# Kernel tuning notes

Hardware: AMD Instinct MI355X
Metric: run time of the kernel (lower is better)

The kernel has to match this reference:

```python
import jax, jax.numpy as jnp
import numpy as np
from jax import lax

EDGES = [(11,12),(11,23),(12,24),(23,24),(23,25),(25,27),(24,26),(26,28),(11,13),(13,15),(12,14),(14,16)]
J = 33

def _build_neighbors():
    nb = [[j] for j in range(J)]
    for a, b in EDGES:
        nb[a].append(b); nb[b].append(a)
    K = max(len(n) for n in nb)
    idx = np.zeros((J, K), np.int32)
    msk = np.zeros((J, K), np.float32)
    for j, n in enumerate(nb):
        idx[j, :len(n)] = n; msk[j, :len(n)] = 1.0
    return jnp.asarray(idx), jnp.asarray(msk)

NBR_IDX, NBR_MASK = _build_neighbors()
BN_EPS = 1e-5

def conv(x, w, b):
    y = lax.conv_general_dilated(x, w, (1, 1), 'SAME', dimension_numbers=('NCHW', 'OIHW', 'NCHW'))
    return y + b[None, :, None, None]

def bn(x, g, b):
    # eval-mode BatchNorm with running_mean=0, running_var=1
    s = g / jnp.sqrt(1.0 + BN_EPS)
    return x * s[None, :, None, None] + b[None, :, None, None]

def maxpool2(x):
    return lax.reduce_window(x, -jnp.inf, lax.max, (1, 1, 2, 2), (1, 1, 2, 2), 'VALID')

def deconv2x2(x, w, b):
    # ConvTranspose2d(k=2, s=2): w is [Cin, Cout, 2, 2]
    y = jnp.einsum('bcij,codk->boidjk', x, w)
    B, O, H, _, W, _ = y.shape
    return y.reshape(B, O, 2 * H, 2 * W) + b[None, :, None, None]

def forward(x, conv1_w, conv1_b, bn1_g, bn1_b, conv2_w, conv2_b, bn2_g, bn2_b,
            conv3_w, conv3_b, bn3_g, bn3_b, conv4_w, conv4_b, bn4_g, bn4_b,
            dc1_w, dc1_b, dc2_w, dc2_b, head_w, head_b, proj_w, proj_b,
            msg_w, msg_b, gru_w_ih, gru_w_hh, gru_b_ih, gru_b_hh,
            refine_w, refine_b, vis_w1, vis_b1, vis_w2, vis_b2):
    relu = jax.nn.relu
    h = bn(relu(conv(x, conv1_w, conv1_b)), bn1_g, bn1_b)
    h = bn(relu(conv(h, conv2_w, conv2_b)), bn2_g, bn2_b)
    h = maxpool2(h)
    h = bn(relu(conv(h, conv3_w, conv3_b)), bn3_g, bn3_b)
    h = maxpool2(h)
    enc = bn(relu(conv(h, conv4_w, conv4_b)), bn4_g, bn4_b)  # [B,256,H/4,W/4]
    f = relu(deconv2x2(enc, dc1_w, dc1_b))
    feat_map = relu(deconv2x2(f, dc2_w, dc2_b))  # [B,64,H,W]
    init_hm = jax.nn.sigmoid(conv(feat_map, head_w, head_b))  # [B,J,H,W]
    B, Jn, H, W = init_hm.shape
    sm = jax.nn.softmax(init_hm.reshape(B, Jn, H * W) / 0.1, axis=-1).reshape(B, Jn, H, W)
    w_idx = jnp.linspace(0.0, 1.0, W)
    h_idx = jnp.linspace(0.0, 1.0, H)
    pred_x = (sm.sum(-2) * w_idx).sum(-1)  # [B,J] in [0,1]
    pred_y = (sm.sum(-1) * h_idx).sum(-1)
    # grid_sample bilinear, align_corners=True: grid=(2p-1) -> pixel coord p*(dim-1)
    ix = pred_x * (W - 1)
    iy = pred_y * (H - 1)
    x0 = jnp.clip(jnp.floor(ix), 0, W - 1)
    y0 = jnp.clip(jnp.floor(iy), 0, H - 1)
    wx = ix - x0
    wy = iy - y0
    x0i = x0.astype(jnp.int32); x1i = jnp.clip(x0i + 1, 0, W - 1)
    y0i = y0.astype(jnp.int32); y1i = jnp.clip(y0i + 1, 0, H - 1)
    fm = feat_map.transpose(0, 2, 3, 1)  # [B,H,W,C]
    bidx = jnp.arange(B)[:, None]
    v00 = fm[bidx, y0i, x0i]; v01 = fm[bidx, y0i, x1i]
    v10 = fm[bidx, y1i, x0i]; v11 = fm[bidx, y1i, x1i]
    wx = wx[..., None]; wy = wy[..., None]
    joint = (v00 * (1 - wx) * (1 - wy) + v01 * wx * (1 - wy)
             + v10 * (1 - wx) * wy + v11 * wx * wy)  # [B,J,64]
    joint_feats = joint @ proj_w.T + proj_b
    # SkeletonGNN (all joints read original joint_feats -> fully parallel)
    gathered = joint_feats[:, NBR_IDX, :]  # [B,J,K,D]
    lin = gathered @ msg_w.T + msg_b
    m = NBR_MASK[None, :, :, None]
    msgs = (lin * m).sum(2) / NBR_MASK.sum(1)[None, :, None]  # [B,J,D]
    gi = msgs @ gru_w_ih.T + gru_b_ih
    gh = joint_feats @ gru_w_hh.T + gru_b_hh
    D = joint_feats.shape[-1]
    ir, iz, inn = gi[..., :D], gi[..., D:2 * D], gi[..., 2 * D:]
    hr, hz, hn = gh[..., :D], gh[..., D:2 * D], gh[..., 2 * D:]
    r = jax.nn.sigmoid(ir + hr)
    z = jax.nn.sigmoid(iz + hz)
    n = jnp.tanh(inn + r * hn)
    refined_feats = (1 - z) * n + z * joint_feats
    refined_bias = refined_feats.mean(-1)[:, :, None, None]
    refined_hm = jax.nn.sigmoid(conv(init_hm, refine_w, refine_b) + refined_bias)
    # visibility head: adaptive avg pool to 4x4 (enc HW divisible by 4), eval dropout = identity
    eB, eC, eH, eW = enc.shape
    p = enc.reshape(eB, eC, 4, eH // 4, 4, eW // 4).mean((3, 5))  # [B,256,4,4]
    v = jax.nn.relu(p.reshape(eB, -1) @ vis_w1.T + vis_b1)
    vis_pred = jax.nn.sigmoid(v @ vis_w2.T + vis_b2)
    return refined_hm, vis_pred

def setup_inputs() -> dict:
    key = jax.random.key(0)
    ks = iter(jax.random.split(key, 64))
    def w(shape, s=0.05):
        return (jax.random.normal(next(ks), shape, dtype=jnp.float32) * s)
    inp = {
        'x': jax.random.normal(next(ks), (16, 3, 256, 256), dtype=jnp.float32),
        'conv1_w': w((32, 3, 3, 3)), 'conv1_b': w((32,)), 'bn1_g': jnp.ones((32,)), 'bn1_b': jnp.zeros((32,)),
        'conv2_w': w((64, 32, 3, 3)), 'conv2_b': w((64,)), 'bn2_g': jnp.ones((64,)), 'bn2_b': jnp.zeros((64,)),
        'conv3_w': w((128, 64, 3, 3)), 'conv3_b': w((128,)), 'bn3_g': jnp.ones((128,)), 'bn3_b': jnp.zeros((128,)),
        'conv4_w': w((256, 128, 3, 3)), 'conv4_b': w((256,)), 'bn4_g': jnp.ones((256,)), 'bn4_b': jnp.zeros((256,)),
        'dc1_w': w((256, 128, 2, 2)), 'dc1_b': w((128,)),
        'dc2_w': w((128, 64, 2, 2)), 'dc2_b': w((64,)),
        'head_w': w((33, 64, 1, 1)), 'head_b': w((33,)),
        'proj_w': w((64, 64)), 'proj_b': w((64,)),
        'msg_w': w((64, 64)), 'msg_b': w((64,)),
        'gru_w_ih': w((192, 64)), 'gru_w_hh': w((192, 64)),
        'gru_b_ih': w((192,)), 'gru_b_hh': w((192,)),
        'refine_w': w((33, 33, 3, 3)), 'refine_b': w((33,)),
        'vis_w1': w((256, 256 * 16)), 'vis_b1': w((256,)),
        'vis_w2': w((33, 256)), 'vis_b2': w((33,)),
    }
    return inp

def reference(x, conv1_w, conv1_b, bn1_g, bn1_b, conv2_w, conv2_b, bn2_g, bn2_b,
              conv3_w, conv3_b, bn3_g, bn3_b, conv4_w, conv4_b, bn4_g, bn4_b,
              dc1_w, dc1_b, dc2_w, dc2_b, head_w, head_b, proj_w, proj_b,
              msg_w, msg_b, gru_w_ih, gru_w_hh, gru_b_ih, gru_b_hh,
              refine_w, refine_b, vis_w1, vis_b1, vis_w2, vis_b2):
    return forward(x, conv1_w, conv1_b, bn1_g, bn1_b, conv2_w, conv2_b, bn2_g, bn2_b,
                   conv3_w, conv3_b, bn3_g, bn3_b, conv4_w, conv4_b, bn4_g, bn4_b,
                   dc1_w, dc1_b, dc2_w, dc2_b, head_w, head_b, proj_w, proj_b,
                   msg_w, msg_b, gru_w_ih, gru_w_hh, gru_b_ih, gru_b_hh,
                   refine_w, refine_b, vis_w1, vis_b1, vis_w2, vis_b2)
```

## Files before the change

### kernel.cpp

```cpp
#include <hip/hip_runtime.h>
#include <hip/hip_bf16.h>
#include <math.h>

#define BN_RS 0.99999500003749977f

typedef __attribute__((ext_vector_type(8))) __bf16 bf16x8;
typedef __attribute__((ext_vector_type(4))) float f32x4;

union U16 { uint4 u; bf16x8 v; __hip_bfloat16 h[8]; };
union U8  { uint2 u; __hip_bfloat16 h[4]; };

__device__ __forceinline__ float sigf(float v) { return 1.0f / (1.0f + expf(-v)); }

__global__ __launch_bounds__(256)
void repack_conv_w_k(const float* __restrict__ w, __hip_bfloat16* __restrict__ wb,
                     int taps, int Co, int Ci, int CoT, int Kp)
{
    int i = blockIdx.x * 256 + threadIdx.x;
    int tot = taps * CoT * Kp;
    if (i >= tot) return;
    int k = i % Kp, n = (i / Kp) % CoT, t = i / (Kp * CoT);
    float v = (n < Co && k < Ci) ? w[((long)n * Ci + k) * taps + t] : 0.0f;
    wb[i] = __float2bfloat16(v);
}
__global__ __launch_bounds__(256)
void repack_conv_w_ilv_k(const float* __restrict__ w, __hip_bfloat16* __restrict__ wb,
                         int taps, int Co, int Ci, int CoT, int Kp)
{
    int i = blockIdx.x * 256 + threadIdx.x;
    int tot = taps * CoT * Kp;
    if (i >= tot) return;
    int k = i % Kp, n = (i / Kp) % CoT, t = i / (Kp * CoT);
    int grp = n >> 6, r = n & 63;
    int c = (grp << 6) + (r & 15) * 4 + (r >> 4);
    float v = (c < Co && k < Ci) ? w[((long)c * Ci + k) * taps + t] : 0.0f;
    wb[i] = __float2bfloat16(v);
}
__global__ __launch_bounds__(256)
void repack_deconv_w_ilv_k(const float* __restrict__ w, __hip_bfloat16* __restrict__ wb,
                           int Co, int Ci)
{
    int i = blockIdx.x * 256 + threadIdx.x;
    int tot = 4 * Co * Ci;
    if (i >= tot) return;
    int k = i % Ci, n = (i / Ci) % Co, q = i / (Ci * Co);
    int grp = n >> 6, r = n & 63;
    int c = (grp << 6) + (r & 15) * 4 + (r >> 4);
    wb[i] = __float2bfloat16(w[((long)k * Co + c) * 4 + q]);
}

__global__ __launch_bounds__(256)
void zero_halo_k(__hip_bfloat16* __restrict__ buf, int H, int W, int C, int B)
{
    const int P = W + 2;
    const long per = (long)(2 * P + 2 * H) * C;
    long idx = (long)blockIdx.x * 256 + threadIdx.x;
    if (idx >= per * B) return;
    int b = (int)(idx / per);
    long r = idx % per;
    long off;
    if (r < (long)2 * P * C) {
        int row = (r >= (long)P * C) ? (H + 1) : 0;
        long r2 = r % ((long)P * C);
        off = (((long)b * (H + 2) + row) * P) * C + r2;
    } else {
        long r2 = r - (long)2 * P * C;
        int row = 1 + (int)(r2 / (2 * C));
        int side = (int)((r2 / C) & 1);
        int ch = (int)(r2 % C);
        off = (((long)b * (H + 2) + row) * P + (side ? (W + 1) : 0)) * C + ch;
    }
    buf[off] = __float2bfloat16(0.0f);
}

__global__ __launch_bounds__(256)
void conv1_k(const float* __restrict__ x, const float* __restrict__ w,
             const float* __restrict__ cb, const float* __restrict__ g,
             const float* __restrict__ bb, __hip_bfloat16* __restrict__ out)
{
    __shared__ float sw[216];
    const int tid = threadIdx.x;
    const int b = blockIdx.z >> 2, cg = blockIdx.z & 3, co0 = cg * 8;
    for (int i = tid; i < 216; i += 256) {
        int t = i % 9, co = (i / 9) % 8, ci = i / 72;
        sw[i] = w[((co0 + co) * 3 + ci) * 9 + t];
    }
    __syncthreads();
    const int tx = tid & 15, ty = tid >> 4;
    const int y = blockIdx.y * 16 + ty;
    const int xs = blockIdx.x * 64 + tx;
    float acc[4][8];
#pragma unroll
    for (int p = 0; p < 4; ++p)
#pragma unroll
        for (int c = 0; c < 8; ++c) acc[p][c] = 0.0f;
    for (int ci = 0; ci < 3; ++ci) {
        const float* plane = x + ((long)b * 3 + ci) * 65536;
#pragma unroll
        for (int t = 0; t < 9; ++t) {
            const int dy = t / 3 - 1, dx = t % 3 - 1;
            const int yy = y + dy;
            if ((unsigned)yy < 256u) {
                const float* row = plane + yy * 256;
                float wsr[8];
#pragma unroll
                for (int c = 0; c < 8; ++c) wsr[c] = sw[ci * 72 + c * 9 + t];
#pragma unroll
                for (int p = 0; p < 4; ++p) {
                    const int xx = xs + p * 16 + dx;
                    const float v = ((unsigned)xx < 256u) ? row[xx] : 0.0f;
#pragma unroll
                    for (int c = 0; c < 8; ++c) acc[p][c] = fmaf(v, wsr[c], acc[p][c]);
                }
            }
        }
    }
#pragma unroll
    for (int p = 0; p < 4; ++p) {
        U16 o;
#pragma unroll
        for (int c = 0; c < 8; ++c) {
            const int cc = co0 + c;
            float v = fmaxf(acc[p][c] + cb[cc], 0.0f) * (g[cc] * BN_RS) + bb[cc];
            o.h[c] = __float2bfloat16(v);
        }
        *(uint4*)(void*)(out + ((long)b * 2130048L + ((long)y * 258 + xs + p * 16) * 32) + co0) = o.u;
    }
}

template<int MI>
__global__ __launch_bounds__(256)
void mfma_conv_k(const __hip_bfloat16* __restrict__ in,
                 const __hip_bfloat16* __restrict__ wb,
                 const float* __restrict__ cbias,
                 const float* __restrict__ bng, const float* __restrict__ bnb,
                 __hip_bfloat16* __restrict__ out_bf,
                 int H, int W, int Cin, int PIT, long bstride, long obstride, int OPIT,
                 int CoutT, int CG, int S)
{
    const int tid = threadIdx.x;
    const int wid = tid >> 6, lane = tid & 63;
    const int ln = lane & 15, kg = lane >> 4;
    const int nx = gridDim.x;
    const int bx = (blockIdx.x & 7) * (nx >> 3) + (blockIdx.x >> 3);
    const int u = bx * 4 + wid;
    const int y = u / S, x0 = (u % S) * (MI * 16);
    const int b = blockIdx.z / CG, cg = blockIdx.z % CG;
    const int co0 = cg * 64;
    const int KC = Cin >> 5;

    f32x4 acc[MI][4];
#pragma unroll
    for (int i = 0; i < MI; ++i)
#pragma unroll
        for (int j = 0; j < 4; ++j) acc[i][j] = f32x4{0.f, 0.f, 0.f, 0.f};

    for (int kc = 0; kc < KC; ++kc) {
        const int kofs = kc * 32 + kg * 8;
#pragma unroll
        for (int t = 0; t < 9; ++t) {
            const int dy = t / 3 - 1, dx = t % 3 - 1;
            bf16x8 wfr[4];
#pragma unroll
            for (int ni = 0; ni < 4; ++ni)
                wfr[ni] = *(const bf16x8*)(const void*)(wb + ((long)t * CoutT + co0 + ni * 16 + ln) * Cin + kofs);
            U16 av[MI];
            const long rowb = (long)b * bstride + (long)(y + dy) * PIT * Cin + kofs;
#pragma unroll
            for (int mi = 0; mi < MI; ++mi)
                av[mi].u = *(const uint4*)(const void*)(in + rowb + (long)(x0 + mi * 16 + ln + dx) * Cin);
#pragma unroll
            for (int mi = 0; mi < MI; ++mi)
#pragma unroll
                for (int ni = 0; ni < 4; ++ni)
                    acc[mi][ni] = __builtin_amdgcn_mfma_f32_16x16x32_bf16(av[mi].v, wfr[ni], acc[mi][ni], 0, 0, 0);
        }
    }
#pragma unroll
    for (int mi = 0; mi < MI; ++mi) {
#pragma unroll
        for (int r = 0; r < 4; ++r) {
            const int px = x0 + mi * 16 + kg * 4 + r;
            const long pb = (long)b * obstride + ((long)y * OPIT + px) * CoutT + co0;
            U8 o;
#pragma unroll
            for (int ni = 0; ni < 4; ++ni) {
                const int c = co0 + ln * 4 + ni;
                float v = acc[mi][ni][r] + cbias[c];
                v = fmaxf(v, 0.0f) * (bng[c] * BN_RS) + bnb[c];
                o.h[ni] = __float2bfloat16(v);
            }
            *(uint2*)(void*)(out_bf + pb + ln * 4) = o.u;
        }
    }
}

__global__ __launch_bounds__(256)
void mfma_deconv_k(const __hip_bfloat16* __restrict__ in,
                   const __hip_bfloat16* __restrict__ wb,
                   const float* __restrict__ bias,
                   __hip_bfloat16* __restrict__ out,
                   int H, int W, int Cin, int CoutT, int CG, int S)
{
    const int tid = threadIdx.x;
    const int wid = tid >> 6, lane = tid & 63;
    const int ln = lane & 15, kg = lane >> 4;
    const int nx = gridDim.x;
    const int bx = (blockIdx.x & 7) * (nx >> 3) + (blockIdx.x >> 3);
    const int u = bx * 4 + wid;
    const int y = u / S, x0 = (u % S) * 32;
    const int b = blockIdx.z / CG, cg = blockIdx.z % CG;
    const int co0 = cg * 64;
    const int KC = Cin >> 5;
    const long inb = (long)b * H * W * Cin;
    const int W2 = W * 2;
    const long ob = (long)b * 4 * H * W * CoutT;

    for (int q = 0; q < 4; ++q) {
        const int dy = q >> 1, dx = q & 1;
        f32x4 acc[2][4];
#pragma unroll
        for (int i = 0; i < 2; ++i)
#pragma unroll
            for (int j = 0; j < 4; ++j) acc[i][j] = f32x4{0.f, 0.f, 0.f, 0.f};
        for (int kc = 0; kc < KC; ++kc) {
            const int kofs = kc * 32 + kg * 8;
            bf16x8 wfr[4];
            U16 av[2];
#pragma unroll
            for (int ni = 0; ni < 4; ++ni)
                wfr[ni] = *(const bf16x8*)(const void*)(wb + ((long)q * CoutT + co0 + ni * 16 + ln) * Cin + kofs);
#pragma unroll
            for (int mi = 0; mi < 2; ++mi)
                av[mi].u = *(const uint4*)(const void*)(in + inb + ((long)y * W + x0 + mi * 16 + ln) * Cin + kofs);
#pragma unroll
            for (int mi = 0; mi < 2; ++mi)
#pragma unroll
                for (int ni = 0; ni < 4; ++ni)
                    acc[mi][ni] = __builtin_amdgcn_mfma_f32_16x16x32_bf16(av[mi].v, wfr[ni], acc[mi][ni], 0, 0, 0);
        }
#pragma unroll
        for (int mi = 0; mi < 2; ++mi) {
#pragma unroll
            for (int r = 0; r < 4; ++r) {
                const int xl = x0 + mi * 16 + kg * 4 + r;
                const long pb = ob + ((long)(2 * y + dy) * W2 + 2 * xl + dx) * CoutT + co0;
                U8 o;
#pragma unroll
                for (int ni = 0; ni < 4; ++ni) {
                    const int c = co0 + ln * 4 + ni;
                    float v = fmaxf(acc[mi][ni][r] + bias[c], 0.0f);
                    o.h[ni] = __float2bfloat16(v);
                }
                *(uint2*)(void*)(out + pb + ln * 4) = o.u;
            }
        }
    }
}

__global__ __launch_bounds__(256)
void mfma_head_k(const __hip_bfloat16* __restrict__ in,
                 const __hip_bfloat16* __restrict__ wb,
                 const float* __restrict__ hb,
                 __hip_bfloat16* __restrict__ out)
{
    const int tid = threadIdx.x;
    const int wid = tid >> 6, lane = tid & 63;
    const int ln = lane & 15, kg = lane >> 4;
    const int nx = gridDim.x;
    const int bx = (blockIdx.x & 7) * (nx >> 3) + (blockIdx.x >> 3);
    const int u = bx * 4 + wid;
    const int y = u >> 3, x0 = (u & 7) * 32;
    const int b = blockIdx.z;

    f32x4 acc[2][4];
#pragma unroll
    for (int i = 0; i < 2; ++i)
#pragma unroll
        for (int j = 0; j < 4; ++j) acc[i][j] = f32x4{0.f, 0.f, 0.f, 0.f};

    for (int kc = 0; kc < 2; ++kc) {
        const int kofs = kc * 32 + kg * 8;
        bf16x8 wfr[4];
#pragma unroll
        for (int ni = 0; ni < 4; ++ni)
            wfr[ni] = *(const bf16x8*)(const void*)(wb + ((long)(ni * 16 + ln)) * 64 + kofs);
        U16 av[2];
#pragma unroll
        for (int mi = 0; mi < 2; ++mi)
            av[mi].u = *(const uint4*)(const void*)(in + (long)b * 4194304L + ((long)y * 256 + x0 + mi * 16 + ln) * 64 + kofs);
#pragma unroll
        for (int mi = 0; mi < 2; ++mi)
#pragma unroll
            for (int ni = 0; ni < 4; ++ni)
                acc[mi][ni] = __builtin_amdgcn_mfma_f32_16x16x32_bf16(av[mi].v, wfr[ni], acc[mi][ni], 0, 0, 0);
    }
#pragma unroll
    for (int mi = 0; mi < 2; ++mi) {
#pragma unroll
        for (int r = 0; r < 4; ++r) {
            const int px = x0 + mi * 16 + kg * 4 + r;
            const long pb = (long)b * 4260096L + ((long)y * 258 + px) * 64;
            U8 o;
#pragma unroll
            for (int ni = 0; ni < 4; ++ni) {
                const int c = ln * 4 + ni;
                float v = (c < 33) ? sigf(acc[mi][ni][r] + hb[c]) : 0.0f;
                o.h[ni] = __float2bfloat16(v);
            }
            *(uint2*)(void*)(out + pb + ln * 4) = o.u;
        }
    }
}

__global__ __launch_bounds__(256)
void mfma_refine_k(const __hip_bfloat16* __restrict__ in,
                   const __hip_bfloat16* __restrict__ wb,
                   const float* __restrict__ cbias, const float* __restrict__ ebias,
                   float* __restrict__ out_f32)
{
    extern __shared__ float ltr[];
    const int tid = threadIdx.x;
    const int wid = tid >> 6, lane = tid & 63;
    const int ln = lane & 15, kg = lane >> 4;
    const int nx = gridDim.x;
    const int bx = (blockIdx.x & 7) * (nx >> 3) + (blockIdx.x >> 3);
    const int u = bx * 4 + wid;
    const int y = u >> 3, x0 = (u & 7) * 32;
    const int b = blockIdx.z;

    f32x4 acc[2][3];
#pragma unroll
    for (int i = 0; i < 2; ++i)
#pragma unroll
        for (int j = 0; j < 3; ++j) acc[i][j] = f32x4{0.f, 0.f, 0.f, 0.f};

    for (int kc = 0; kc < 2; ++kc) {
        const int kofs = kc * 32 + kg * 8;
#pragma unroll
        for (int t = 0; t < 9; ++t) {
            const int dy = t / 3 - 1, dx = t % 3 - 1;
            bf16x8 wfr[3];
#pragma unroll
            for (int ni = 0; ni < 3; ++ni)
                wfr[ni] = *(const bf16x8*)(const void*)(wb + ((long)t * 64 + ni * 16 + ln) * 64 + kofs);
            U16 av[2];
            const long rowb = (long)b * 4260096L + (long)(y + dy) * 258 * 64 + kofs;
#pragma unroll
            for (int mi = 0; mi < 2; ++mi)
                av[mi].u = *(const uint4*)(const void*)(in + rowb + (long)(x0 + mi * 16 + ln + dx) * 64);
#pragma unroll
            for (int mi = 0; mi < 2; ++mi)
#pragma unroll
                for (int ni = 0; ni < 3; ++ni)
                    acc[mi][ni] = __builtin_amdgcn_mfma_f32_16x16x32_bf16(av[mi].v, wfr[ni], acc[mi][ni], 0, 0, 0);
        }
    }

    float* wt = ltr + wid * 1680;
#pragma unroll
    for (int mi = 0; mi < 2; ++mi) {
#pragma unroll
        for (int r = 0; r < 4; ++r) {
            const int pxl = mi * 16 + kg * 4 + r;
#pragma unroll
            for (int ni = 0; ni < 3; ++ni) {
                const int c = ni * 16 + ln;
                float eb = (c < 33) ? (cbias[c] + ebias[b * 33 + c]) : 0.0f;
                wt[c * 35 + pxl] = sigf(acc[mi][ni][r] + eb);
            }
        }
    }
    __syncthreads();
    const int yb = (bx * 4) >> 3;
    const int xb = ((bx * 4) & 7) * 32;
    const int coff = bx % 33;
    for (int i = tid; i < 4224; i += 256) {
        int cl = i >> 7, p = i & 127;
        int c = cl + coff; if (c >= 33) c -= 33;
        float v = ltr[(p >> 5) * 1680 + c * 35 + (p & 31)];
        out_f32[((long)b * 33 + c) * 65536L + (long)yb * 256 + xb + p] = v;
    }
}

__global__ __launch_bounds__(256)
void maxpool_bf_k(const __hip_bfloat16* __restrict__ in, __hip_bfloat16* __restrict__ out,
                  int Ho, int Wo, int C, long total, int OPIT, long obstride)
{
    long idx = (long)blockIdx.x * 256 + threadIdx.x;
    if (idx >= total) return;
    const int ng = C >> 3;
    const int cg = (int)(idx % ng);
    long pix = idx / ng;
    const int xo = (int)(pix % Wo); pix /= Wo;
    const int yo = (int)(pix % Ho);
    const int b = (int)(pix / Ho);
    const int Wi = Wo * 2;
    const __hip_bfloat16* p = in + (((long)b * 2 * Ho + 2 * yo) * Wi + 2 * xo) * C + cg * 8;
    U16 a0, a1, a2, a3, o;
    a0.u = *(const uint4*)(const void*)p;
    a1.u = *(const uint4*)(const void*)(p + C);
    a2.u = *(const uint4*)(const void*)(p + (long)Wi * C);
    a3.u = *(const uint4*)(const void*)(p + (long)Wi * C + C);
#pragma unroll
    for (int j = 0; j < 8; ++j) {
        float m = fmaxf(fmaxf(__bfloat162float(a0.h[j]), __bfloat162float(a1.h[j])),
                        fmaxf(__bfloat162float(a2.h[j]), __bfloat162float(a3.h[j])));
        o.h[j] = __float2bfloat16(m);
    }
    *(uint4*)(void*)(out + (long)b * obstride + ((long)yo * OPIT + xo) * C + cg * 8) = o.u;
}

__global__ __launch_bounds__(256)
void softargmax_nhwc_k(const __hip_bfloat16* __restrict__ hd, float* __restrict__ coords)
{
    __shared__ float sm[8][256];
    __shared__ float fin[8][4];
    const int b = blockIdx.x, jg = blockIdx.y;
    const int tid = threadIdx.x;
    const __hip_bfloat16* base = hd + (long)b * 4260096L + jg * 8;
    float m[8];
#pragma unroll
    for (int c = 0; c < 8; ++c) m[c] = -1e30f;
    for (int i = tid; i < 65536; i += 256) {
        int y = i >> 8, x = i & 255;
        U16 v; v.u = *(const uint4*)(const void*)(base + ((long)y * 258 + x) * 64);
#pragma unroll
        for (int c = 0; c < 8; ++c) m[c] = fmaxf(m[c], __bfloat162float(v.h[c]));
    }
#pragma unroll
    for (int c = 0; c < 8; ++c) sm[c][tid] = m[c];
    __syncthreads();
    for (int s = 128; s > 0; s >>= 1) {
        if (tid < s)
#pragma unroll
            for (int c = 0; c < 8; ++c) sm[c][tid] = fmaxf(sm[c][tid], sm[c][tid + s]);
        __syncthreads();
    }
    if (tid < 8) fin[tid][0] = sm[tid][0];
    __syncthreads();
#pragma unroll
    for (int c = 0; c < 8; ++c) m[c] = fin[c][0];
    float s8[8], sx8[8], sy8[8];
#pragma unroll
    for (int c = 0; c < 8; ++c) { s8[c] = 0.f; sx8[c] = 0.f; sy8[c] = 0.f; }
    for (int i = tid; i < 65536; i += 256) {
        int y = i >> 8, x = i & 255;
        U16 v; v.u = *(const uint4*)(const void*)(base + ((long)y * 258 + x) * 64);
#pragma unroll
        for (int c = 0; c < 8; ++c) {
            float e = expf((__bfloat162float(v.h[c]) - m[c]) * 10.0f);
            s8[c] += e; sx8[c] += e * (float)x; sy8[c] += e * (float)y;
        }
    }
    for (int which = 0; which < 3; ++which) {
        __syncthreads();
#pragma unroll
        for (int c = 0; c < 8; ++c)
            sm[c][tid] = (which == 0) ? s8[c] : (which == 1) ? sx8[c] : sy8[c];
        __syncthreads();
        for (int s = 128; s > 0; s >>= 1) {
            if (tid < s)
#pragma unroll
                for (int c = 0; c < 8; ++c) sm[c][tid] += sm[c][tid + s];
            __syncthreads();
        }
        if (tid < 8) fin[tid][1 + which] = sm[tid][0];
    }
    __syncthreads();
    if (tid < 8) {
        int j = jg * 8 + tid;
        if (j < 33) {
            coords[2 * (b * 33 + j)]     = fin[tid][2] / fin[tid][1];
            coords[2 * (b * 33 + j) + 1] = fin[tid][3] / fin[tid][1];
        }
    }
}

__global__ __launch_bounds__(64)
void joint_bf_k(const __hip_bfloat16* __restrict__ fm, const float* __restrict__ coords,
                const float* __restrict__ pw, const float* __restrict__ pb,
                float* __restrict__ jf)
{
    __shared__ float sj[64];
    const int bj = blockIdx.x, b = bj / 33;
    const int tid = threadIdx.x;
    float ix = coords[2 * bj], iy = coords[2 * bj + 1];
    float x0f = fminf(fmaxf(floorf(ix), 0.0f), 255.0f);
    float y0f = fminf(fmaxf(floorf(iy), 0.0f), 255.0f);
    float wx = ix - x0f, wy = iy - y0f;
    int x0 = (int)x0f, y0 = (int)y0f;
    int x1 = min(x0 + 1, 255), y1 = min(y0 + 1, 255);
    const __hip_bfloat16* base = fm + (long)b * 65536 * 64 + tid;
    float v00 = __bfloat162float(base[((long)y0 * 256 + x0) * 64]);
    float v01 = __bfloat162float(base[((long)y0 * 256 + x1) * 64]);
    float v10 = __bfloat162float(base[((long)y1 * 256 + x0) * 64]);
    float v11 = __bfloat162float(base[((long)y1 * 256 + x1) * 64]);
    sj[tid] = v00 * (1 - wx) * (1 - wy) + v01 * wx * (1 - wy)
            + v10 * (1 - wx) * wy + v11 * wx * wy;
    __syncthreads();
    float a = pb[tid];
    for (int k = 0; k < 64; ++k) a = fmaf(sj[k], pw[tid * 64 + k], a);
    jf[(long)bj * 64 + tid] = a;
}

__device__ const int d_nbr[33][4] = {
    {0,0,0,0},{1,0,0,0},{2,0,0,0},{3,0,0,0},{4,0,0,0},{5,0,0,0},{6,0,0,0},{7,0,0,0},
    {8,0,0,0},{9,0,0,0},{10,0,0,0},
    {11,12,23,13},{12,11,24,14},{13,11,15,0},{14,12,16,0},{15,13,0,0},{16,14,0,0},
    {17,0,0,0},{18,0,0,0},{19,0,0,0},{20,0,0,0},{21,0,0,0},{22,0,0,0},
    {23,11,24,25},{24,12,23,26},{25,23,27,0},{26,24,28,0},{27,25,0,0},{28,26,0,0},
    {29,0,0,0},{30,0,0,0},{31,0,0,0},{32,0,0,0}};
__device__ const int d_cnt[33] = {1,1,1,1,1,1,1,1,1,1,1,4,4,3,3,2,2,1,1,1,1,1,1,4,4,3,3,2,2,1,1,1,1};

__global__ __launch_bounds__(192)
void gru_k(const float* __restrict__ jf, const float* __restrict__ mw, const float* __restrict__ mb,
           const float* __restrict__ wih, const float* __restrict__ whh,
           const float* __restrict__ bih, const float* __restrict__ bhh,
           float* __restrict__ rbias)
{
    __shared__ float s_mjf[64], s_jf[64], s_msg[64], s_gi[192], s_gh[192], s_ref[64];
    const int bj = blockIdx.x;
    const int b = bj / 33, j = bj % 33;
    const int tid = threadIdx.x;
    if (tid < 64) {
        int cnt = d_cnt[j];
        float s = 0.0f;
        for (int n = 0; n < 4; ++n)
            if (n < cnt) s += jf[((long)b * 33 + d_nbr[j][n]) * 64 + tid];
        s_mjf[tid] = s / (float)cnt;
        s_jf[tid] = jf[(long)bj * 64 + tid];
    }
    __syncthreads();
    if (tid < 64) {
        float a = mb[tid];
        for (int k = 0; k < 64; ++k) a = fmaf(mw[tid * 64 + k], s_mjf[k], a);
        s_msg[tid] = a;
    }
    __syncthreads();
    {
        float a = bih[tid], c = bhh[tid];
        for (int k = 0; k < 64; ++k) {
            a = fmaf(wih[tid * 64 + k], s_msg[k], a);
            c = fmaf(whh[tid * 64 + k], s_jf[k], c);
        }
        s_gi[tid] = a; s_gh[tid] = c;
    }
    __syncthreads();
    if (tid < 64) {
        float r = sigf(s_gi[tid] + s_gh[tid]);
        float z = sigf(s_gi[64 + tid] + s_gh[64 + tid]);
        float n = tanhf(s_gi[128 + tid] + r * s_gh[128 + tid]);
        s_ref[tid] = (1.0f - z) * n + z * s_jf[tid];
    }
    __syncthreads();
    if (tid == 0) {
        float s = 0.0f;
        for (int k = 0; k < 64; ++k) s += s_ref[k];
        rbias[bj] = s * (1.0f / 64.0f);
    }
}

__global__ __launch_bounds__(256)
void vispool_bf_k(const __hip_bfloat16* __restrict__ enc, float* __restrict__ p)
{
    int idx = blockIdx.x * 256 + threadIdx.x;
    int v = idx & 3, uu = (idx >> 2) & 3, c = (idx >> 4) & 255, b = idx >> 12;
    const __hip_bfloat16* base = enc + (long)b * 64 * 64 * 256 + c;
    float s = 0.0f;
    for (int a = 0; a < 16; ++a)
#pragma unroll
        for (int d = 0; d < 16; ++d)
            s += __bfloat162float(base[((long)(uu * 16 + a) * 64 + (v * 16 + d)) * 256]);
    p[idx] = s * (1.0f / 256.0f);
}

__global__ __launch_bounds__(256)
void visfc1_k(const float* __restrict__ p, const float* __restrict__ w1,
              const float* __restrict__ b1, float* __restrict__ v1)
{
    __shared__ float s_p[4096];
    const int b = blockIdx.x, tid = threadIdx.x;
    for (int i = tid; i < 4096; i += 256) s_p[i] = p[b * 4096 + i];
    __syncthreads();
    float a = b1[tid];
    const float* wr = w1 + (long)tid * 4096;
    for (int k = 0; k < 4096; ++k) a = fmaf(wr[k], s_p[k], a);
    v1[b * 256 + tid] = fmaxf(a, 0.0f);
}

__global__ __launch_bounds__(64)
void visfc2_k(const float* __restrict__ v1, const float* __restrict__ w2,
              const float* __restrict__ b2, float* __restrict__ out)
{
    const int b = blockIdx.x, t = threadIdx.x;
    if (t < 33) {
        float a = b2[t];
        for (int k = 0; k < 256; ++k) a = fmaf(w2[t * 256 + k], v1[b * 256 + k], a);
        out[b * 33 + t] = sigf(a);
    }
}

extern "C" void kernel_launch(void* const* d_in, const int* in_sizes, int n_in,
                              void* d_out, int out_size, void* d_ws, size_t ws_size,
                              hipStream_t stream)
{
    const float* x   = (const float*)d_in[0];
    const float* c1w = (const float*)d_in[1];  const float* c1b = (const float*)d_in[2];
    const float* b1g = (const float*)d_in[3];  const float* b1b = (const float*)d_in[4];
    const float* c2w = (const float*)d_in[5];  const float* c2b = (const float*)d_in[6];
    const float* b2g = (const float*)d_in[7];  const float* b2b = (const float*)d_in[8];
    const float* c3w = (const float*)d_in[9];  const float* c3b = (const float*)d_in[10];
    const float* b3g = (const float*)d_in[11]; const float* b3b = (const float*)d_in[12];
    const float* c4w = (const float*)d_in[13]; const float* c4b = (const float*)d_in[14];
    const float* b4g = (const float*)d_in[15]; const float* b4b = (const float*)d_in[16];
    const float* d1w = (const float*)d_in[17]; const float* d1b = (const float*)d_in[18];
    const float* d2w = (const float*)d_in[19]; const float* d2b = (const float*)d_in[20];
    const float* hw  = (const float*)d_in[21]; const float* hb  = (const float*)d_in[22];
    const float* pw  = (const float*)d_in[23]; const float* pb  = (const float*)d_in[24];
    const float* mw  = (const float*)d_in[25]; const float* mb  = (const float*)d_in[26];
    const float* wih = (const float*)d_in[27]; const float* whh = (const float*)d_in[28];
    const float* bih = (const float*)d_in[29]; const float* bhh = (const float*)d_in[30];
    const float* rw  = (const float*)d_in[31]; const float* rb  = (const float*)d_in[32];
    const float* v1w = (const float*)d_in[33]; const float* v1b = (const float*)d_in[34];
    const float* v2w = (const float*)d_in[35]; const float* v2b = (const float*)d_in[36];

    char* ws = (char*)d_ws;
    __hip_bfloat16* ENC  = (__hip_bfloat16*)(ws + 0L);
    __hip_bfloat16* R1   = (__hip_bfloat16*)(ws + 33554432L);
    __hip_bfloat16* R2   = (__hip_bfloat16*)(ws + 167772160L);
    char*           R3c  = ws + 304095232L;
    char* SM = ws + 442507264L;

    __hip_bfloat16* H1B = R1;                 __hip_bfloat16* H1I = R1 + 8288;
    __hip_bfloat16* P1B = R1;                 __hip_bfloat16* P1I = R1 + 8384;
    __hip_bfloat16* FEAT = R1;
    __hip_bfloat16* H3  = R2;
    __hip_bfloat16* F   = R2;
    __hip_bfloat16* HDB = R2;                 __hip_bfloat16* HDI = R2 + 16576;
    __hip_bfloat16* P2B = (__hip_bfloat16*)R3c; __hip_bfloat16* P2I = P2B + 8576;

    __hip_bfloat16* W2B = (__hip_bfloat16*)(SM + 0);
    __hip_bfloat16* W3B = (__hip_bfloat16*)(SM + 36864);
    __hip_bfloat16* W4B = (__hip_bfloat16*)(SM + 184320);
    __hip_bfloat16* WRB = (__hip_bfloat16*)(SM + 774144);
    __hip_bfloat16* WHB = (__hip_bfloat16*)(SM + 847872);
    __hip_bfloat16* WD1 = (__hip_bfloat16*)(SM + 856064);
    __hip_bfloat16* WD2 = (__hip_bfloat16*)(SM + 1118208);
    float* CO = (float*)(SM + 1183744);
    float* JF = (float*)(SM + 1187968);
    float* RB = (float*)(SM + 1323136);
    float* P  = (float*)(SM + 1325248);
    float* V1 = (float*)(SM + 1587392);

    float* out_hm  = (float*)d_out;
    float* out_vis = out_hm + 34603008L;
    __hip_bfloat16* H2 = (__hip_bfloat16*)d_out;

    repack_conv_w_ilv_k<<<(9*64*32 + 255)/256, 256, 0, stream>>>(c2w, W2B, 9, 64, 32, 64, 32);
    repack_conv_w_ilv_k<<<(9*128*64 + 255)/256, 256, 0, stream>>>(c3w, W3B, 9, 128, 64, 128, 64);
    repack_conv_w_ilv_k<<<(9*256*128 + 255)/256, 256, 0, stream>>>(c4w, W4B, 9, 256, 128, 256, 128);
    repack_conv_w_k<<<(9*64*64 + 255)/256, 256, 0, stream>>>(rw, WRB, 9, 33, 33, 64, 64);
    repack_conv_w_ilv_k<<<(1*64*64 + 255)/256, 256, 0, stream>>>(hw, WHB, 1, 33, 64, 64, 64);
    repack_deconv_w_ilv_k<<<(4*128*256 + 255)/256, 256, 0, stream>>>(d1w, WD1, 128, 256);
    repack_deconv_w_ilv_k<<<(4*64*128 + 255)/256, 256, 0, stream>>>(d2w, WD2, 64, 128);

    zero_halo_k<<<(526336 + 255)/256, 256, 0, stream>>>(H1B, 256, 256, 32, 16);
    zero_halo_k<<<(532480 + 255)/256, 256, 0, stream>>>(P2B, 64, 64, 128, 16);

    conv1_k<<<dim3(4, 16, 64), 256, 0, stream>>>(x, c1w, c1b, b1g, b1b, H1I);
    mfma_conv_k<2><<<dim3(512, 1, 16), 256, 0, stream>>>(
        H1I, W2B, c2b, b2g, b2b, H2,
        256, 256, 32, 258, 2130048L, 4194304L, 256, 64, 1, 8);
    zero_halo_k<<<(528384 + 255)/256, 256, 0, stream>>>(P1B, 128, 128, 64, 16);
    maxpool_bf_k<<<8192, 256, 0, stream>>>(H2, P1I, 128, 128, 64, 2097152L, 130, 1081600L);
    mfma_conv_k<2><<<dim3(128, 1, 32), 256, 0, stream>>>(
        P1I, W3B, c3b, b3g, b3b, H3,
        128, 128, 64, 130, 1081600L, 2097152L, 128, 128, 2, 4);
    maxpool_bf_k<<<4096, 256, 0, stream>>>(H3, P2I, 64, 64, 128, 1048576L, 66, 557568L);
    mfma_conv_k<2><<<dim3(32, 1, 64), 256, 0, stream>>>(
        P2I, W4B, c4b, b4g, b4b, ENC,
        64, 64, 128, 66, 557568L, 1048576L, 64, 256, 4, 2);
    mfma_deconv_k<<<dim3(32, 1, 32), 256, 0, stream>>>(
        ENC, WD1, d1b, F, 64, 64, 256, 128, 2, 2);
    mfma_deconv_k<<<dim3(128, 1, 16), 256, 0, stream>>>(
        F, WD2, d2b, FEAT, 128, 128, 128, 64, 1, 4);
    zero_halo_k<<<(1052672 + 255)/256, 256, 0, stream>>>(HDB, 256, 256, 64, 16);
    mfma_head_k<<<dim3(512, 1, 16), 256, 0, stream>>>(FEAT, WHB, hb, HDI);
    softargmax_nhwc_k<<<dim3(16, 5), 256, 0, stream>>>(HDI, CO);
    joint_bf_k<<<528, 64, 0, stream>>>(FEAT, CO, pw, pb, JF);
    gru_k<<<528, 192, 0, stream>>>(JF, mw, mb, wih, whh, bih, bhh, RB);
    mfma_refine_k<<<dim3(512, 1, 16), 256, 26880, stream>>>(
        HDI, WRB, rb, RB, out_hm);
    vispool_bf_k<<<256, 256, 0, stream>>>(ENC, P);
    visfc1_k<<<16, 256, 0, stream>>>(P, v1w, v1b, V1);
    visfc2_k<<<16, 64, 0, stream>>>(V1, v2w, v2b, out_vis);
}
```

Measured before the change: 1.856 ms.

## Split soft-argmax into per-slab partial reductions plus a combine kernel

```diff
diff --git a/kernel.cpp b/kernel.cpp
--- a/kernel.cpp
+++ b/kernel.cpp
@@ -412,69 +412,96 @@
 }
 
 __global__ __launch_bounds__(256)
-void softargmax_nhwc_k(const __hip_bfloat16* __restrict__ hd, float* __restrict__ coords)
-{
-    __shared__ float sm[8][256];
-    __shared__ float fin[8][4];
-    const int b = blockIdx.x, jg = blockIdx.y;
+void softargmax_slab_k(const __hip_bfloat16* __restrict__ hd, float* __restrict__ ss)
+{
+    __shared__ float sm[64 * 33];
+    __shared__ float mg[64];
+    const int blk = blockIdx.x;
+    const int b = blk >> 4, slab = blk & 15;
     const int tid = threadIdx.x;
-    const __hip_bfloat16* base = hd + (long)b * 4260096L + jg * 8;
-    float m[8];
-#pragma unroll
-    for (int c = 0; c < 8; ++c) m[c] = -1e30f;
-    for (int i = tid; i < 65536; i += 256) {
-        int y = i >> 8, x = i & 255;
-        U16 v; v.u = *(const uint4*)(const void*)(base + ((long)y * 258 + x) * 64);
-#pragma unroll
-        for (int c = 0; c < 8; ++c) m[c] = fmaxf(m[c], __bfloat162float(v.h[c]));
-    }
-#pragma unroll
-    for (int c = 0; c < 8; ++c) sm[c][tid] = m[c];
-    __syncthreads();
-    for (int s = 128; s > 0; s >>= 1) {
-        if (tid < s)
-#pragma unroll
-            for (int c = 0; c < 8; ++c) sm[c][tid] = fmaxf(sm[c][tid], sm[c][tid + s]);
+    const int pxl = tid >> 3, cg = tid & 7;
+    const __hip_bfloat16* base = hd + (long)b * 4260096L + (long)(slab * 16) * 258 * 64 + cg * 8;
+
+    float m8[8];
+#pragma unroll
+    for (int c = 0; c < 8; ++c) m8[c] = -1e30f;
+    for (int yy = 0; yy < 16; ++yy)
+        for (int xc = 0; xc < 8; ++xc) {
+            U16 v; v.u = *(const uint4*)(const void*)(base + ((long)yy * 258 + xc * 32 + pxl) * 64);
+#pragma unroll
+            for (int c = 0; c < 8; ++c) m8[c] = fmaxf(m8[c], __bfloat162float(v.h[c]));
+        }
+#pragma unroll
+    for (int c = 0; c < 8; ++c) sm[(cg * 8 + c) * 33 + pxl] = m8[c];
+    __syncthreads();
+    for (int s = 16; s > 0; s >>= 1) {
+        if (pxl < s)
+#pragma unroll
+            for (int c = 0; c < 8; ++c) {
+                int a = (cg * 8 + c) * 33;
+                sm[a + pxl] = fmaxf(sm[a + pxl], sm[a + pxl + s]);
+            }
         __syncthreads();
     }
-    if (tid < 8) fin[tid][0] = sm[tid][0];
-    __syncthreads();
-#pragma unroll
-    for (int c = 0; c < 8; ++c) m[c] = fin[c][0];
+    if (tid < 64) mg[tid] = sm[tid * 33];
+    __syncthreads();
+    if (tid < 33) ss[(long)blk * 132 + tid] = mg[tid];
+    float mm[8];
+#pragma unroll
+    for (int c = 0; c < 8; ++c) mm[c] = mg[cg * 8 + c];
+
     float s8[8], sx8[8], sy8[8];
 #pragma unroll
     for (int c = 0; c < 8; ++c) { s8[c] = 0.f; sx8[c] = 0.f; sy8[c] = 0.f; }
-    for (int i = tid; i < 65536; i += 256) {
-        int y = i >> 8, x = i & 255;
-        U16 v; v.u = *(const uint4*)(const void*)(base + ((long)y * 258 + x) * 64);
-#pragma unroll
-        for (int c = 0; c < 8; ++c) {
-            float e = expf((__bfloat162float(v.h[c]) - m[c]) * 10.0f);
-            s8[c] += e; sx8[c] += e * (float)x; sy8[c] += e * (float)y;
+    for (int yy = 0; yy < 16; ++yy) {
+        const float fy = (float)(slab * 16 + yy);
+        for (int xc = 0; xc < 8; ++xc) {
+            const int x = xc * 32 + pxl;
+            U16 v; v.u = *(const uint4*)(const void*)(base + ((long)yy * 258 + x) * 64);
+#pragma unroll
+            for (int c = 0; c < 8; ++c) {
+                float e = expf((__bfloat162float(v.h[c]) - mm[c]) * 10.0f);
+                s8[c] += e; sx8[c] += e * (float)x; sy8[c] += e * fy;
+            }
         }
     }
     for (int which = 0; which < 3; ++which) {
         __syncthreads();
 #pragma unroll
         for (int c = 0; c < 8; ++c)
-            sm[c][tid] = (which == 0) ? s8[c] : (which == 1) ? sx8[c] : sy8[c];
+            sm[(cg * 8 + c) * 33 + pxl] = (which == 0) ? s8[c] : (which == 1) ? sx8[c] : sy8[c];
         __syncthreads();
-        for (int s = 128; s > 0; s >>= 1) {
-            if (tid < s)
-#pragma unroll
-                for (int c = 0; c < 8; ++c) sm[c][tid] += sm[c][tid + s];
+        for (int s = 16; s > 0; s >>= 1) {
+            if (pxl < s)
+#pragma unroll
+                for (int c = 0; c < 8; ++c) {
+                    int a = (cg * 8 + c) * 33;
+                    sm[a + pxl] += sm[a + pxl + s];
+                }
             __syncthreads();
         }
-        if (tid < 8) fin[tid][1 + which] = sm[tid][0];
-    }
-    __syncthreads();
-    if (tid < 8) {
-        int j = jg * 8 + tid;
-        if (j < 33) {
-            coords[2 * (b * 33 + j)]     = fin[tid][2] / fin[tid][1];
-            coords[2 * (b * 33 + j) + 1] = fin[tid][3] / fin[tid][1];
-        }
-    }
+        if (tid < 33) ss[(long)blk * 132 + (which + 1) * 33 + tid] = sm[tid * 33];
+    }
+}
+
+__global__ __launch_bounds__(64)
+void softargmax_comb_k(const float* __restrict__ ss, float* __restrict__ coords)
+{
+    const int b = blockIdx.x, j = threadIdx.x;
+    if (j >= 33) return;
+    float mg = -1e30f;
+    for (int sl = 0; sl < 16; ++sl)
+        mg = fmaxf(mg, ss[(long)(b * 16 + sl) * 132 + j]);
+    float S = 0.f, SX = 0.f, SY = 0.f;
+    for (int sl = 0; sl < 16; ++sl) {
+        const long o = (long)(b * 16 + sl) * 132;
+        float sc = expf((ss[o + j] - mg) * 10.0f);
+        S  += ss[o + 33 + j] * sc;
+        SX += ss[o + 66 + j] * sc;
+        SY += ss[o + 99 + j] * sc;
+    }
+    coords[2 * (b * 33 + j)]     = SX / S;
+    coords[2 * (b * 33 + j) + 1] = SY / S;
 }
 
 __global__ __launch_bounds__(64)
@@ -652,6 +679,7 @@
     float* RB = (float*)(SM + 1323136);
     float* P  = (float*)(SM + 1325248);
     float* V1 = (float*)(SM + 1587392);
+    float* SS = (float*)(SM + 1603840);
 
     float* out_hm  = (float*)d_out;
     float* out_vis = out_hm + 34603008L;
@@ -687,7 +715,8 @@
         F, WD2, d2b, FEAT, 128, 128, 128, 64, 1, 4);
     zero_halo_k<<<(1052672 + 255)/256, 256, 0, stream>>>(HDB, 256, 256, 64, 16);
     mfma_head_k<<<dim3(512, 1, 16), 256, 0, stream>>>(FEAT, WHB, hb, HDI);
-    softargmax_nhwc_k<<<dim3(16, 5), 256, 0, stream>>>(HDI, CO);
+    softargmax_slab_k<<<256, 256, 0, stream>>>(HDI, SS);
+    softargmax_comb_k<<<16, 64, 0, stream>>>(SS, CO);
     joint_bf_k<<<528, 64, 0, stream>>>(FEAT, CO, pw, pb, JF);
     gru_k<<<528, 192, 0, stream>>>(JF, mw, mb, wih, whh, bih, bhh, RB);
     mfma_refine_k<<<dim3(512, 1, 16), 256, 26880, stream>>>(
```

New measurement: 1.623 ms. 1.14x faster.
